# Kernel tuning notes

Hardware: AMD Instinct MI355X
Metric: run time of the kernel (lower is better)

The kernel has to match this reference:

```python
import jax, jax.numpy as jnp
import numpy as np

# torch mode -> jnp.pad mode: reflect->'reflect', replicate->'edge', circular->'wrap'
# Input layout: [N, C, H, W]. torch 4-tuple pads act on (W, H); 6-tuple pads act on (W, H, C).

def setup_inputs() -> dict:
    key = jax.random.key(0)
    x = jax.random.normal(key, (16, 32, 512, 512), dtype=jnp.float32)
    return {"x": x}


def _pad_chain(x):
    # 1) F.pad(x, (1,1,0,0), 'reflect')      -> W +-1
    x = jnp.pad(x, ((0, 0), (0, 0), (0, 0), (1, 1)), mode="reflect")
    # 2) F.pad(x, (0,0,2,2), 'reflect')      -> H +-2
    x = jnp.pad(x, ((0, 0), (0, 0), (2, 2), (0, 0)), mode="reflect")
    # 3) F.pad(x, (0,0,2,2), 'replicate')    -> H +-2 (edge)
    x = jnp.pad(x, ((0, 0), (0, 0), (2, 2), (0, 0)), mode="edge")
    # 4) F.pad(x, (0,0,0,0,1,1), 'circular') -> C +-1 (wrap)
    x = jnp.pad(x, ((0, 0), (1, 1), (0, 0), (0, 0)), mode="wrap")
    # 5) F.pad(x, (0,0,0,0,3,3), 'circular') -> C +-3 (wrap)
    x = jnp.pad(x, ((0, 0), (3, 3), (0, 0), (0, 0)), mode="wrap")
    # 6) F.pad(x, (1,1,3,0,0,3), 'replicate')-> W +-1, H +3 front, C +3 back
    x = jnp.pad(x, ((0, 0), (0, 3), (3, 0), (1, 1)), mode="edge")
    # 7) F.pad(x, (1,1,3,0,0,3), 'reflect')  -> W +-1, H +3 front, C +3 back
    x = jnp.pad(x, ((0, 0), (0, 3), (3, 0), (1, 1)), mode="reflect")
    return x


def reference(x) -> jnp.ndarray:
    return _pad_chain(x)
```

## Files before the change

kernel.cpp:

```cpp
#include <hip/hip_runtime.h>


__device__ __forceinline__ int hmap(int d) {
    if (d <= 8)   return 2;
    if (d == 9)   return 1;
    if (d <= 521) return d - 10;
    return (d == 522) ? 510 : 509;
}

__device__ __forceinline__ int cmap(int g) {
    if (g >= 43) g = 84 - g;
    if (g > 39)  g = 39;
    int p = g - 3;
    if (p < 0)   p += 34;
    if (p >= 34) p -= 34;
    return (p == 0) ? 31 : ((p <= 32) ? (p - 1) : 0);
}

__global__ __launch_bounds__(256) void pad_rows_kernel(const float* __restrict__ x,
                                                       float* __restrict__ out) {
    const int nc = blockIdx.y;
    const int c  = nc % 46;
    const int n  = nc / 46;
    const int ci = cmap(c);

    const int half = threadIdx.x >> 7;
    const int tt   = threadIdx.x & 127;
    const int h    = (blockIdx.x << 1) | half;
    const int hi   = hmap(h);

    const float* in_row  = x   + ((((size_t)n * 32 + ci) * 512 + hi) << 9);
    float*       out_row = out + ((size_t)nc * 526 + h) * 518;

    const float4 v = reinterpret_cast<const float4*>(in_row)[tt];
    *reinterpret_cast<float4*>(out_row + 3 + (tt << 2)) = v;

    if (tt == 0) {
        const float e = in_row[1];
        out_row[0] = e; out_row[1] = e; out_row[2] = e;
    } else if (tt == 127) {
        const float e = v.z;
        out_row[515] = e; out_row[516] = e; out_row[517] = e;
    }
}

extern "C" void kernel_launch(void* const* d_in, const int* in_sizes, int n_in,
                              void* d_out, int out_size, void* d_ws, size_t ws_size,
                              hipStream_t stream) {
    const float* x = (const float*)d_in[0];
    float* out = (float*)d_out;
    dim3 grid(263, 736);
    pad_rows_kernel<<<grid, 256, 0, stream>>>(x, out);
}
```

Baseline: 296.9 us.

## Flatten grid, process two rows per wave with nontemporal stores

```diff
diff --git a/kernel.cpp b/kernel.cpp
--- a/kernel.cpp
+++ b/kernel.cpp
@@ -1,5 +1,7 @@
 #include <hip/hip_runtime.h>
 
+
+using f4 = __attribute__((ext_vector_type(4))) float;
 
 __device__ __forceinline__ int hmap(int d) {
     if (d <= 8)   return 2;
@@ -19,28 +21,49 @@
 
 __global__ __launch_bounds__(256) void pad_rows_kernel(const float* __restrict__ x,
                                                        float* __restrict__ out) {
-    const int nc = blockIdx.y;
-    const int c  = nc % 46;
-    const int n  = nc / 46;
-    const int ci = cmap(c);
+    const int lane = threadIdx.x & 63;
+    const int grp  = threadIdx.x >> 6;
+    const int rowA = blockIdx.x * 8 + grp * 2;
+    const int rowB = rowA + 1;
 
-    const int half = threadIdx.x >> 7;
-    const int tt   = threadIdx.x & 127;
-    const int h    = (blockIdx.x << 1) | half;
-    const int hi   = hmap(h);
+    const int ncA = rowA / 526;
+    const int hA  = rowA - ncA * 526;
+    const int cA  = ncA % 46;
+    const int nA  = ncA / 46;
+    const int ncB = rowB / 526;
+    const int hB  = rowB - ncB * 526;
+    const int cB  = ncB % 46;
+    const int nB  = ncB / 46;
 
-    const float* in_row  = x   + ((((size_t)n * 32 + ci) * 512 + hi) << 9);
-    float*       out_row = out + ((size_t)nc * 526 + h) * 518;
+    const float* inA = x + ((((size_t)nA * 32 + cmap(cA)) * 512 + hmap(hA)) << 9);
+    const float* inB = x + ((((size_t)nB * 32 + cmap(cB)) * 512 + hmap(hB)) << 9);
+    float* outA = out + (size_t)rowA * 518;
+    float* outB = out + (size_t)rowB * 518;
 
-    const float4 v = reinterpret_cast<const float4*>(in_row)[tt];
-    *reinterpret_cast<float4*>(out_row + 3 + (tt << 2)) = v;
+    const f4 a0 = reinterpret_cast<const f4*>(inA)[2 * lane];
+    const f4 a1 = reinterpret_cast<const f4*>(inA)[2 * lane + 1];
+    const f4 b0 = reinterpret_cast<const f4*>(inB)[2 * lane];
+    const f4 b1 = reinterpret_cast<const f4*>(inB)[2 * lane + 1];
 
-    if (tt == 0) {
-        const float e = in_row[1];
-        out_row[0] = e; out_row[1] = e; out_row[2] = e;
-    } else if (tt == 127) {
-        const float e = v.z;
-        out_row[515] = e; out_row[516] = e; out_row[517] = e;
+    __builtin_nontemporal_store(a0, reinterpret_cast<f4*>(outA + 3 + 8 * lane));
+    __builtin_nontemporal_store(a1, reinterpret_cast<f4*>(outA + 7 + 8 * lane));
+    __builtin_nontemporal_store(b0, reinterpret_cast<f4*>(outB + 3 + 8 * lane));
+    __builtin_nontemporal_store(b1, reinterpret_cast<f4*>(outB + 7 + 8 * lane));
+
+    if (lane == 0) {
+        __builtin_nontemporal_store(a0.y, outA + 0);
+        __builtin_nontemporal_store(a0.y, outA + 1);
+        __builtin_nontemporal_store(a0.y, outA + 2);
+        __builtin_nontemporal_store(b0.y, outB + 0);
+        __builtin_nontemporal_store(b0.y, outB + 1);
+        __builtin_nontemporal_store(b0.y, outB + 2);
+    } else if (lane == 63) {
+        __builtin_nontemporal_store(a1.z, outA + 515);
+        __builtin_nontemporal_store(a1.z, outA + 516);
+        __builtin_nontemporal_store(a1.z, outA + 517);
+        __builtin_nontemporal_store(b1.z, outB + 515);
+        __builtin_nontemporal_store(b1.z, outB + 516);
+        __builtin_nontemporal_store(b1.z, outB + 517);
     }
 }
 
@@ -49,6 +72,5 @@
                               hipStream_t stream) {
     const float* x = (const float*)d_in[0];
     float* out = (float*)d_out;
-    dim3 grid(263, 736);
-    pad_rows_kernel<<<grid, 256, 0, stream>>>(x, out);
+    pad_rows_kernel<<<48392, 256, 0, stream>>>(x, out);
 }
```

Result: slower. 386.9 us (+30.3%).
